# Performance work log

Hardware: AMD Instinct MI355X
Metric: run time of the kernel (lower is better)

The kernel has to match this reference:

```python
import jax, jax.numpy as jnp
import numpy as np

INPUT, HIDDEN = 15, 20

def setup_inputs() -> dict:
    key = jax.random.key(0)
    k1, k2, k3, k4, k5 = jax.random.split(key, 5)
    B, T = 4096, 512
    s = 1.0 / np.sqrt(HIDDEN)  # torch default uniform init bound
    feature = jax.random.normal(k1, (B, T, INPUT), dtype=jnp.float32)
    W_ih = jax.random.uniform(k2, (HIDDEN, INPUT), jnp.float32, -s, s)
    W_hh = jax.random.uniform(k3, (HIDDEN, HIDDEN), jnp.float32, -s, s)
    b_ih = jax.random.uniform(k4, (HIDDEN,), jnp.float32, -s, s)
    b_hh = jax.random.uniform(k5, (HIDDEN,), jnp.float32, -s, s)
    return {"feature": feature, "W_ih": W_ih, "W_hh": W_hh, "b_ih": b_ih, "b_hh": b_hh}

def reference(feature, W_ih, W_hh, b_ih, b_hh):
    # h_t = tanh(x_t @ W_ih^T + b_ih + h_{t-1} @ W_hh^T + b_hh)
    B, T, _ = feature.shape
    # precompute input projections for all timesteps: [T, B, H]
    xp = jnp.einsum('bti,hi->tbh', feature, W_ih) + (b_ih + b_hh)
    h0 = jnp.zeros((B, HIDDEN), dtype=feature.dtype)
    def step(h, x_t):
        h_new = jnp.tanh(x_t + h @ W_hh.T)
        return h_new, None
    hn, _ = jax.lax.scan(step, h0, xp)
    return hn  # [B, H] == hn.squeeze() for num_layers=1
```

## Files before the change

### kernel.cpp

```cpp
#include <hip/hip_runtime.h>
#include <cstddef>


typedef float f4 __attribute__((ext_vector_type(4)));
typedef float g4 __attribute__((ext_vector_type(4), aligned(4)));
typedef _Float16 h2 __attribute__((ext_vector_type(2)));
typedef _Float16 v4h __attribute__((ext_vector_type(4)));
typedef _Float16 v8h __attribute__((ext_vector_type(8)));
typedef __fp16 p2 __attribute__((ext_vector_type(2)));

#define TT 512
#define IN 15
#define HD 20
#define NB 16

__device__ __forceinline__ float fexp2(float x) {
#if __has_builtin(__builtin_amdgcn_exp2f)
  return __builtin_amdgcn_exp2f(x);
#else
  return exp2f(x);
#endif
}
__device__ __forceinline__ h2 pk2(float a, float b) {
  p2 r = __builtin_amdgcn_cvt_pkrtz(a, b);
  return __builtin_bit_cast(h2, r);
}
__device__ __forceinline__ v4h cat4(h2 a, h2 b) {
  return __builtin_shufflevector(a, b, 0, 1, 2, 3);
}
__device__ __forceinline__ v8h cat8(v4h a, v4h b) {
  return __builtin_shufflevector(a, b, 0, 1, 2, 3, 4, 5, 6, 7);
}

__global__ __launch_bounds__(64) void rnn_mfma(
    const float* __restrict__ feature, const float* __restrict__ W_ih,
    const float* __restrict__ W_hh, const float* __restrict__ b_ih,
    const float* __restrict__ b_hh, float* __restrict__ out, int B) {
  const int l = threadIdx.x;
  const int G = l >> 4;
  const int mf = l & 15;
  const int b0 = blockIdx.x * NB;

  const float K2 = 2.8853900817779268f;

  const int jPa = 8 * (mf >> 2) + (mf & 3);
  const int jQa = jPa + 4;

  v8h AhhP, AhhQ;
#pragma unroll
  for (int i = 0; i < 8; ++i) {
    const int k = 8 * G + i;
    AhhP[i] = (_Float16)((jPa < HD && k < HD) ? K2 * W_hh[jPa * HD + k] : 0.f);
    AhhQ[i] = (_Float16)((jQa < HD && k < HD) ? K2 * W_hh[jQa * HD + k] : 0.f);
  }
  const int k0 = (G < 3) ? 4 * G : 11;
  v4h AihP, AihQ;
#pragma unroll
  for (int i = 0; i < 4; ++i) {
    const int k = k0 + i;
    const bool dup = (G == 2 && i == 3);
    AihP[i] = (_Float16)((jPa < HD && k < IN && !dup) ? K2 * W_ih[jPa * IN + k]
                                                      : 0.f);
    AihQ[i] = (_Float16)((jQa < HD && k < IN && !dup) ? K2 * W_ih[jQa * IN + k]
                                                      : 0.f);
  }
  f4 biasP, biasQ;
#pragma unroll
  for (int r = 0; r < 4; ++r) {
    const int jp = 8 * G + r, jq = jp + 4;
    biasP[r] = (jp < HD) ? K2 * (b_ih[jp] + b_hh[jp]) : 0.f;
    biasQ[r] = (jq < HD) ? K2 * (b_ih[jq] + b_hh[jq]) : 0.f;
  }

  const int b = min(b0 + mf, B - 1);
  const float* xbase = feature + (size_t)b * TT * IN + k0;
  auto load_x = [&](int t) -> g4 {
    return *(const g4*)(xbase + (size_t)t * IN);
  };

  g4 XR[8];
#pragma unroll
  for (int s = 1; s <= 8; ++s) XR[s & 7] = load_x(s);

  g4 x0 = load_x(0);
  v4h X0 = cat4(pk2(x0.x, x0.y), pk2(x0.z, x0.w));
  f4 cxPc = __builtin_amdgcn_mfma_f32_16x16x16f16(AihP, X0, biasP, 0, 0, 0);
  f4 cxQc = __builtin_amdgcn_mfma_f32_16x16x16f16(AihQ, X0, biasQ, 0, 0, 0);

  v8h Bh;
#pragma unroll
  for (int i = 0; i < 8; ++i) Bh[i] = (_Float16)0.f;

  float tPk[4], tQk[4];

  for (int t = 0; t < TT; t += 8) {
#pragma unroll
    for (int u = 0; u < 8; ++u) {
      f4 aP = __builtin_amdgcn_mfma_f32_16x16x32_f16(AhhP, Bh, cxPc, 0, 0, 0);
      f4 aQ = __builtin_amdgcn_mfma_f32_16x16x32_f16(AhhQ, Bh, cxQc, 0, 0, 0);
      const int s = (u + 1) & 7;
      g4 xr = XR[s];
      v4h Xn = cat4(pk2(xr.x, xr.y), pk2(xr.z, xr.w));
      cxPc = __builtin_amdgcn_mfma_f32_16x16x16f16(AihP, Xn, biasP, 0, 0, 0);
      cxQc = __builtin_amdgcn_mfma_f32_16x16x16f16(AihQ, Xn, biasQ, 0, 0, 0);
      const int tn = t + u + 9;
      XR[s] = load_x(tn < TT ? tn : TT - 1);
#pragma unroll
      for (int r = 0; r < 4; ++r) {
        const float eP = fexp2(aP[r]);
        tPk[r] = 1.f - 2.f * __builtin_amdgcn_rcpf(1.f + eP);
        const float eQ = fexp2(aQ[r]);
        tQk[r] = 1.f - 2.f * __builtin_amdgcn_rcpf(1.f + eQ);
      }
      Bh = cat8(cat4(pk2(tPk[0], tPk[1]), pk2(tPk[2], tPk[3])),
                cat4(pk2(tQk[0], tQk[1]), pk2(tQk[2], tQk[3])));
    }
  }

  const int batch = b0 + mf;
  if (batch < B) {
    float* orow = out + (size_t)batch * HD;
#pragma unroll
    for (int r = 0; r < 4; ++r) {
      const int jp = 8 * G + r;
      if (jp < HD) orow[jp] = tPk[r];
      const int jq = jp + 4;
      if (jq < HD) orow[jq] = tQk[r];
    }
  }
}

extern "C" void kernel_launch(void* const* d_in, const int* in_sizes, int n_in,
                              void* d_out, int out_size, void* d_ws, size_t ws_size,
                              hipStream_t stream) {
  const float* feature = (const float*)d_in[0];
  const float* W_ih    = (const float*)d_in[1];
  const float* W_hh    = (const float*)d_in[2];
  const float* b_ih    = (const float*)d_in[3];
  const float* b_hh    = (const float*)d_in[4];
  float* out = (float*)d_out;
  const int B = in_sizes[0] / (TT * IN);
  const int grid = (B + NB - 1) / NB;
  rnn_mfma<<<grid, 64, 0, stream>>>(feature, W_ih, W_hh, b_ih, b_hh, out, B);
}
```

Before: 230.3 us.

## Fold tanh affine into weights and compact hidden layout to 5-stride

Rewrites tanh(a) as 1-2*sigmoid-like u, folding the -2 scale into W_hh and the constant term into the bias via W_hh row sums, so the recurrent loop carries u directly. It also remaps the hidden rows into a 5-per-group layout so only 5 of 8 accumulator outputs per lane need the exp/rcp activation. This aims to shorten the per-step serial chain after the MFMA. Risk: fp16 precision of the -2-scaled weights and of u may differ from before.

```diff
diff --git a/kernel.cpp b/kernel.cpp
--- a/kernel.cpp
+++ b/kernel.cpp
@@ -43,15 +43,17 @@
 
   const float K2 = 2.8853900817779268f;
 
-  const int jPa = 8 * (mf >> 2) + (mf & 3);
-  const int jQa = jPa + 4;
+  const int jP = 5 * (mf >> 2) + (mf & 3);
+  const int jQ = 5 * (mf >> 2) + 4;
 
   v8h AhhP, AhhQ;
 #pragma unroll
   for (int i = 0; i < 8; ++i) {
-    const int k = 8 * G + i;
-    AhhP[i] = (_Float16)((jPa < HD && k < HD) ? K2 * W_hh[jPa * HD + k] : 0.f);
-    AhhQ[i] = (_Float16)((jQa < HD && k < HD) ? K2 * W_hh[jQa * HD + k] : 0.f);
+    const int k = 5 * G + i;
+    const float wP = (i < 5) ? -2.f * K2 * W_hh[jP * HD + k] : 0.f;
+    const float wQ = (i < 5) ? -2.f * K2 * W_hh[jQ * HD + k] : 0.f;
+    AhhP[i] = (_Float16)wP;
+    AhhQ[i] = (_Float16)wQ;
   }
   const int k0 = (G < 3) ? 4 * G : 11;
   v4h AihP, AihQ;
@@ -59,17 +61,21 @@
   for (int i = 0; i < 4; ++i) {
     const int k = k0 + i;
     const bool dup = (G == 2 && i == 3);
-    AihP[i] = (_Float16)((jPa < HD && k < IN && !dup) ? K2 * W_ih[jPa * IN + k]
-                                                      : 0.f);
-    AihQ[i] = (_Float16)((jQa < HD && k < IN && !dup) ? K2 * W_ih[jQa * IN + k]
-                                                      : 0.f);
+    AihP[i] = (_Float16)((k < IN && !dup) ? K2 * W_ih[jP * IN + k] : 0.f);
+    AihQ[i] = (_Float16)((k < IN && !dup) ? K2 * W_ih[jQ * IN + k] : 0.f);
   }
   f4 biasP, biasQ;
 #pragma unroll
   for (int r = 0; r < 4; ++r) {
-    const int jp = 8 * G + r, jq = jp + 4;
-    biasP[r] = (jp < HD) ? K2 * (b_ih[jp] + b_hh[jp]) : 0.f;
-    biasQ[r] = (jq < HD) ? K2 * (b_ih[jq] + b_hh[jq]) : 0.f;
+    const int jp = 5 * G + r, jq = 5 * G + 4;
+    float rsP = 0.f, rsQ = 0.f;
+#pragma unroll
+    for (int k = 0; k < HD; ++k) {
+      rsP += W_hh[jp * HD + k];
+      rsQ += W_hh[jq * HD + k];
+    }
+    biasP[r] = K2 * (b_ih[jp] + b_hh[jp] + rsP);
+    biasQ[r] = K2 * (b_ih[jq] + b_hh[jq] + rsQ);
   }
 
   const int b = min(b0 + mf, B - 1);
@@ -89,9 +95,13 @@
 
   v8h Bh;
 #pragma unroll
-  for (int i = 0; i < 8; ++i) Bh[i] = (_Float16)0.f;
+  for (int i = 0; i < 8; ++i) Bh[i] = (_Float16)((i < 5) ? 0.5f : 0.f);
 
-  float tPk[4], tQk[4];
+  float uP[4], uQ0 = 0.5f;
+#pragma unroll
+  for (int r = 0; r < 4; ++r) uP[r] = 0.5f;
+
+  const h2 zero2 = {(_Float16)0.f, (_Float16)0.f};
 
   for (int t = 0; t < TT; t += 8) {
 #pragma unroll
@@ -106,14 +116,11 @@
       const int tn = t + u + 9;
       XR[s] = load_x(tn < TT ? tn : TT - 1);
 #pragma unroll
-      for (int r = 0; r < 4; ++r) {
-        const float eP = fexp2(aP[r]);
-        tPk[r] = 1.f - 2.f * __builtin_amdgcn_rcpf(1.f + eP);
-        const float eQ = fexp2(aQ[r]);
-        tQk[r] = 1.f - 2.f * __builtin_amdgcn_rcpf(1.f + eQ);
-      }
-      Bh = cat8(cat4(pk2(tPk[0], tPk[1]), pk2(tPk[2], tPk[3])),
-                cat4(pk2(tQk[0], tQk[1]), pk2(tQk[2], tQk[3])));
+      for (int r = 0; r < 4; ++r)
+        uP[r] = __builtin_amdgcn_rcpf(1.f + fexp2(aP[r]));
+      uQ0 = __builtin_amdgcn_rcpf(1.f + fexp2(aQ[0]));
+      Bh = cat8(cat4(pk2(uP[0], uP[1]), pk2(uP[2], uP[3])),
+                cat4(pk2(uQ0, 0.f), zero2));
     }
   }
 
@@ -121,12 +128,8 @@
   if (batch < B) {
     float* orow = out + (size_t)batch * HD;
 #pragma unroll
-    for (int r = 0; r < 4; ++r) {
-      const int jp = 8 * G + r;
-      if (jp < HD) orow[jp] = tPk[r];
-      const int jq = jp + 4;
-      if (jq < HD) orow[jq] = tQk[r];
-    }
+    for (int r = 0; r < 4; ++r) orow[5 * G + r] = 1.f - 2.f * uP[r];
+    orow[5 * G + 4] = 1.f - 2.f * uQ0;
   }
 }
 
```

Result: faster. 209.7 us (-8.9%).
